# Kernel tuning notes

Hardware: AMD Instinct MI355X
Metric: run time of the kernel (lower is better)

The kernel has to match this reference:

```python
import jax, jax.numpy as jnp
import numpy as np

B, S, D_MODEL, H = 2, 2048, 1024, 16
D_K = D_MODEL // H
THETA = 10000.0


def setup_inputs() -> dict:
    key = jax.random.key(0)
    k1, k2, k3 = jax.random.split(key, 3)
    x = jax.random.normal(k1, (B, S, D_MODEL), dtype=jnp.float32)
    token_positions = jnp.tile(jnp.arange(S, dtype=jnp.int32), (B, 1))
    qkv_w = jax.random.normal(k2, (3 * D_MODEL, D_MODEL), dtype=jnp.float32) * (D_MODEL ** -0.5)
    out_w = jax.random.normal(k3, (D_MODEL, D_MODEL), dtype=jnp.float32) * (D_MODEL ** -0.5)
    return {"x": x, "token_positions": token_positions, "qkv_w": qkv_w, "out_w": out_w}


def _apply_rope(t, pos):
    # t: [B, H, S, d_k], pos: [B, S]
    half = D_K // 2
    inv_freq = THETA ** (-jnp.arange(0, half, dtype=jnp.float32) * 2.0 / D_K)  # [half]
    ang = pos.astype(jnp.float32)[:, None, :, None] * inv_freq  # [B,1,S,half]
    cos, sin = jnp.cos(ang), jnp.sin(ang)
    t1 = t[..., 0::2]
    t2 = t[..., 1::2]
    r1 = t1 * cos - t2 * sin
    r2 = t1 * sin + t2 * cos
    # interleave back: [..., half, 2] -> [..., d_k]
    return jnp.stack([r1, r2], axis=-1).reshape(t.shape)


def reference(x, token_positions, qkv_w, out_w):
    # fused QKV projection (no bias)
    qkv = jnp.einsum('bsd,ed->bse', x, qkv_w)  # [B,S,3*D_MODEL]
    qkv = qkv.reshape(B, S, 3, H, D_K)
    q = jnp.transpose(qkv[:, :, 0], (0, 2, 1, 3))  # [B,H,S,d_k]
    k = jnp.transpose(qkv[:, :, 1], (0, 2, 1, 3))
    v = jnp.transpose(qkv[:, :, 2], (0, 2, 1, 3))
    q = _apply_rope(q, token_positions)
    k = _apply_rope(k, token_positions)
    scores = jnp.einsum('bhqd,bhkd->bhqk', q, k) / jnp.sqrt(jnp.asarray(D_K, x.dtype))
    causal = jnp.tril(jnp.ones((S, S), dtype=bool))
    neg_inf = jnp.finfo(scores.dtype).min
    scores = jnp.where(causal, scores, neg_inf)
    attn = jax.nn.softmax(scores, axis=-1)
    out = jnp.einsum('bhqk,bhkd->bhqd', attn, v)  # [B,H,S,d_k]
    out = jnp.transpose(out, (0, 2, 1, 3)).reshape(B, S, D_MODEL)
    return jnp.einsum('bsd,ed->bse', out, out_w)
```

## Files before the change

### kernel.cpp

```cpp
#include <hip/hip_runtime.h>
#include <cstdint>

typedef unsigned short u16;
typedef unsigned int u32;
typedef __attribute__((ext_vector_type(8))) short short8;
typedef __attribute__((ext_vector_type(4))) float f32x4;

static constexpr int Bc = 2, Sc = 2048, DMc = 1024, Hc = 16, DKc = 64;
static constexpr int Mc = Bc * Sc;

__device__ __forceinline__ float b2f(u16 u) { return __uint_as_float((u32)u << 16); }
__device__ __forceinline__ u16 f2b(float f) {
  u32 x = __float_as_uint(f);
  return (u16)((x + 0x7fffu + ((x >> 16) & 1u)) >> 16);
}
__device__ __forceinline__ u32 pack2(float lo, float hi) {
  return (u32)f2b(lo) | ((u32)f2b(hi) << 16);
}

__global__ __launch_bounds__(256)
void cvt_f32_bf16_k(const float* __restrict__ src, u16* __restrict__ dst, int n8)
{
  const int i = blockIdx.x * 256 + threadIdx.x;
  if (i >= n8) return;
  const float4 a = *(const float4*)(src + (size_t)i * 8);
  const float4 b = *(const float4*)(src + (size_t)i * 8 + 4);
  uint4 o;
  o.x = pack2(a.x, a.y);
  o.y = pack2(a.z, a.w);
  o.z = pack2(b.x, b.y);
  o.w = pack2(b.z, b.w);
  *(uint4*)(dst + (size_t)i * 8) = o;
}

template <typename OutT>
__global__ __launch_bounds__(256, 2)
void gemm_bt128(const u16* __restrict__ A, const u16* __restrict__ W,
                OutT* __restrict__ C, int M, int N, int K)
{
  __shared__ u16 As[128 * 32];
  __shared__ u16 Bs[128 * 32];
  const int t = threadIdx.x;
  const int w = t >> 6, l = t & 63;
  const int wr = w >> 1, wc = w & 1;
  const int l4 = l >> 4, l15 = l & 15;
  const int bm = blockIdx.x, bn = blockIdx.y;

  f32x4 acc[4][4] = {};

  const int rowA = bm * 128, rowB = bn * 128;
  const int sr = l >> 2, sk = (l & 3) * 8;

  for (int k0 = 0; k0 < K; k0 += 32) {
    __syncthreads();
#pragma unroll
    for (int i = 0; i < 2; ++i) {
      const int chunk = i * 4 + w;
      const u16* ga = A + (size_t)(rowA + chunk * 16 + sr) * K + k0 + sk;
      const u16* gb = W + (size_t)(rowB + chunk * 16 + sr) * K + k0 + sk;
      __builtin_amdgcn_global_load_lds((const __attribute__((address_space(1))) void*)ga,
                                       (__attribute__((address_space(3))) void*)(As + chunk * 512), 16, 0, 0);
      __builtin_amdgcn_global_load_lds((const __attribute__((address_space(1))) void*)gb,
                                       (__attribute__((address_space(3))) void*)(Bs + chunk * 512), 16, 0, 0);
    }
    __syncthreads();
    short8 af[4], bf[4];
#pragma unroll
    for (int m = 0; m < 4; ++m)
      af[m] = *(const short8*)(As + (wr * 64 + m * 16 + l15) * 32 + l4 * 8);
#pragma unroll
    for (int n = 0; n < 4; ++n)
      bf[n] = *(const short8*)(Bs + (wc * 64 + n * 16 + l15) * 32 + l4 * 8);
#pragma unroll
    for (int m = 0; m < 4; ++m)
#pragma unroll
      for (int n = 0; n < 4; ++n)
        acc[m][n] = __builtin_amdgcn_mfma_f32_16x16x32_bf16(af[m], bf[n], acc[m][n], 0, 0, 0);
  }

#pragma unroll
  for (int m = 0; m < 4; ++m) {
    const int r0 = rowA + wr * 64 + m * 16 + l4 * 4;
#pragma unroll
    for (int n = 0; n < 4; ++n) {
      const int c0 = rowB + wc * 64 + n * 16 + l15;
#pragma unroll
      for (int r = 0; r < 4; ++r) {
        const float v = acc[m][n][r];
        if constexpr (sizeof(OutT) == 2)
          C[(size_t)(r0 + r) * N + c0] = (OutT)f2b(v);
        else
          C[(size_t)(r0 + r) * N + c0] = (OutT)v;
      }
    }
  }
}

__global__ void rope_table_k(float2* __restrict__ tab)
{
  const int idx = blockIdx.x * 256 + threadIdx.x;
  const int p = idx >> 5, i = idx & 31;
  const float invf = powf(10000.0f, -(float)(2 * i) / 64.0f);
  const float ang = (float)p * invf;
  tab[idx] = make_float2(cosf(ang), sinf(ang));
}

__global__ __launch_bounds__(256)
void rope_reshape_k(const u16* __restrict__ qkv, const int* __restrict__ tokpos,
                    const float2* __restrict__ tab,
                    u16* __restrict__ Q, u16* __restrict__ K, u16* __restrict__ Vt)
{
  __shared__ u16 Vs[64][72];
  const int t = threadIdx.x;
  const int st = blockIdx.x, h = blockIdx.y, b = blockIdx.z;

  {
    const int sl = t >> 2, iq = t & 3;
    const int s = st * 64 + sl;
    const int p = tokpos[b * Sc + s];
    const size_t row = (size_t)(b * Sc + s) * 3 * DMc + h * DKc + iq * 16;
    const size_t orow = ((size_t)(b * Hc + h) * Sc + s) * DKc + iq * 16;
#pragma unroll
    for (int which = 0; which < 2; ++which) {
      const u16* g = qkv + row + which * DMc;
      uint4 va = *(const uint4*)g;
      uint4 vb = *(const uint4*)(g + 8);
      u32 in[8] = {va.x, va.y, va.z, va.w, vb.x, vb.y, vb.z, vb.w};
      const float scale = (which == 0) ? 0.125f : 1.0f;
      u32 ow[8];
#pragma unroll
      for (int j = 0; j < 8; ++j) {
        const float2 cs = tab[p * 32 + iq * 8 + j];
        const float t1 = b2f((u16)(in[j] & 0xffffu));
        const float t2 = b2f((u16)(in[j] >> 16));
        ow[j] = pack2((t1 * cs.x - t2 * cs.y) * scale, (t1 * cs.y + t2 * cs.x) * scale);
      }
      u16* dst = (which == 0 ? Q : K) + orow;
      *(uint4*)dst = make_uint4(ow[0], ow[1], ow[2], ow[3]);
      *(uint4*)(dst + 8) = make_uint4(ow[4], ow[5], ow[6], ow[7]);
    }
  }
#pragma unroll
  for (int it = 0; it < 2; ++it) {
    const int sv = it * 32 + (t >> 3);
    const int d0 = (t & 7) * 8;
    const u16* g = qkv + (size_t)(b * Sc + st * 64 + sv) * 3 * DMc + 2 * DMc + h * DKc + d0;
    *(uint4*)&Vs[sv][d0] = *(const uint4*)g;
  }
  __syncthreads();
  {
    const int d = t >> 2, s0 = (t & 3) * 16;
    u16 tmp[16];
#pragma unroll
    for (int j = 0; j < 16; ++j) tmp[j] = Vs[s0 + j][d];
    u16* dst = Vt + ((size_t)(b * Hc + h) * DKc + d) * Sc + st * 64 + s0;
    *(uint4*)dst = *(const uint4*)tmp;
    *(uint4*)(dst + 8) = *(const uint4*)(tmp + 8);
  }
}

__global__ __launch_bounds__(256, 2)
void attn_k(const u16* __restrict__ Q, const u16* __restrict__ K,
            const u16* __restrict__ Vt, u16* __restrict__ O)
{
  __shared__ u16 Kls[2][64 * 64];
  __shared__ u16 Vls[2][64 * 64];
  __shared__ u16 Psh[4][16 * 64];
  __shared__ float Fsh[4][16];

  const int t = threadIdx.x, w = t >> 6, l = t & 63;
  const int l4 = l >> 4, l15 = l & 15;

  int bid = blockIdx.x + 16 * (blockIdx.y + Hc * blockIdx.z);
  bid = (bid & 7) * 64 + (bid >> 3);
  const int p = bid & 15, h = (bid >> 4) & 15, b = bid >> 8;

  const size_t bh = (size_t)b * Hc + h;
  const u16* Qb = Q + bh * Sc * DKc;
  const u16* Kb = K + bh * Sc * DKc;
  const u16* Vb = Vt + bh * (size_t)DKc * Sc;
  char* Pw = (char*)&Psh[w][0];
  float* Fw = &Fsh[w][0];
  const int swz = (l15 & 7) << 4;

  int srow[2], scol[2];
#pragma unroll
  for (int j = 0; j < 2; ++j) {
    const int e = j * 256 + t;
    srow[j] = e >> 3;
    scol[j] = (((e & 7) * 16) ^ ((srow[j] & 7) << 4)) >> 1;
  }

  auto stage = [&](int buf, int kv0) {
#pragma unroll
    for (int j = 0; j < 2; ++j) {
      const u16* gk = Kb + (size_t)(kv0 + srow[j]) * DKc + scol[j];
      __builtin_amdgcn_global_load_lds((const __attribute__((address_space(1))) void*)gk,
          (__attribute__((address_space(3))) void*)(&Kls[buf][0] + (j * 256 + w * 64) * 8), 16, 0, 0);
    }
#pragma unroll
    for (int j = 0; j < 2; ++j) {
      const u16* gv = Vb + (size_t)srow[j] * Sc + kv0 + scol[j];
      __builtin_amdgcn_global_load_lds((const __attribute__((address_space(1))) void*)gv,
          (__attribute__((address_space(3))) void*)(&Vls[buf][0] + (j * 256 + w * 64) * 8), 16, 0, 0);
    }
  };

#pragma unroll
  for (int seg = 0; seg < 2; ++seg) {
    const int qt = seg ? p : 31 - p;
    const int q0 = qt * 64 + w * 16;
    const int niter = qt + 1;

    const short8 qf0 = *(const short8*)(Qb + (size_t)(q0 + l15) * DKc + l4 * 8);
    const short8 qf1 = *(const short8*)(Qb + (size_t)(q0 + l15) * DKc + 32 + l4 * 8);

    f32x4 o[4] = {};
    float m = -1e30f, lsum = 0.f;

    stage(0, 0);
    for (int it = 0; it < niter; ++it) {
      const int buf = it & 1;
      const int kv0 = it * 64;
      if (it + 1 < niter) {
        stage(buf ^ 1, kv0 + 64);
        asm volatile("s_waitcnt vmcnt(4)" ::: "memory");
      } else {
        asm volatile("s_waitcnt vmcnt(0)" ::: "memory");
      }
      __builtin_amdgcn_s_barrier();

      const char* Kbuf = (const char*)&Kls[buf][0];
      const char* Vbuf = (const char*)&Vls[buf][0];

      f32x4 sc[4];
#pragma unroll
      for (int c = 0; c < 4; ++c) {
        const int rb = (c * 16 + l15) * 128;
        const short8 ka  = *(const short8*)(Kbuf + rb + ((l4 * 16) ^ swz));
        const short8 kb2 = *(const short8*)(Kbuf + rb + ((64 + l4 * 16) ^ swz));
        f32x4 z = {0.f, 0.f, 0.f, 0.f};
        z = __builtin_amdgcn_mfma_f32_16x16x32_bf16(ka, qf0, z, 0, 0, 0);
        z = __builtin_amdgcn_mfma_f32_16x16x32_bf16(kb2, qf1, z, 0, 0, 0);
        sc[c] = z;
      }
      if (kv0 + 63 > q0) {
#pragma unroll
        for (int c = 0; c < 4; ++c) {
          const int kvr = kv0 + c * 16 + l4 * 4;
#pragma unroll
          for (int r = 0; r < 4; ++r)
            if (kvr + r > q0 + l15) sc[c][r] = -1e30f;
        }
      }
      float pmax = -1e30f;
#pragma unroll
      for (int c = 0; c < 4; ++c)
        pmax = fmaxf(pmax, fmaxf(fmaxf(sc[c][0], sc[c][1]), fmaxf(sc[c][2], sc[c][3])));
      pmax = fmaxf(pmax, __shfl_xor(pmax, 16));
      pmax = fmaxf(pmax, __shfl_xor(pmax, 32));
      const float mnew = fmaxf(m, pmax);
      const float fac = __expf(m - mnew);
      float rs = 0.f;
#pragma unroll
      for (int c = 0; c < 4; ++c) {
        const float p0 = __expf(sc[c][0] - mnew);
        const float p1 = __expf(sc[c][1] - mnew);
        const float p2 = __expf(sc[c][2] - mnew);
        const float p3 = __expf(sc[c][3] - mnew);
        rs += (p0 + p1) + (p2 + p3);
        uint2 pk;
        pk.x = pack2(p0, p1);
        pk.y = pack2(p2, p3);
        *(uint2*)(Pw + ((l15 * 128 + c * 32 + l4 * 8) ^ swz)) = pk;
      }
      rs += __shfl_xor(rs, 16);
      rs += __shfl_xor(rs, 32);
      lsum = lsum * fac + rs;
      m = mnew;
      Fw[l15] = fac;
      const f32x4 f4 = *(const f32x4*)&Fw[l4 * 4];
#pragma unroll
      for (int dc = 0; dc < 4; ++dc) {
        o[dc][0] *= f4[0]; o[dc][1] *= f4[1];
        o[dc][2] *= f4[2]; o[dc][3] *= f4[3];
      }
#pragma unroll
      for (int kv2 = 0; kv2 < 2; ++kv2) {
        const short8 pa = *(const short8*)(Pw + ((l15 * 128 + kv2 * 64 + l4 * 16) ^ swz));
#pragma unroll
        for (int dc = 0; dc < 4; ++dc) {
          const short8 vf = *(const short8*)(Vbuf + (dc * 16 + l15) * 128 + ((kv2 * 64 + l4 * 16) ^ swz));
          o[dc] = __builtin_amdgcn_mfma_f32_16x16x32_bf16(pa, vf, o[dc], 0, 0, 0);
        }
      }
      asm volatile("s_waitcnt lgkmcnt(0)" ::: "memory");
      __builtin_amdgcn_s_barrier();
    }
    Fw[l15] = lsum;
    const f32x4 lv = *(const f32x4*)&Fw[l4 * 4];
#pragma unroll
    for (int dc = 0; dc < 4; ++dc) {
      const int col = h * DKc + dc * 16 + l15;
#pragma unroll
      for (int r = 0; r < 4; ++r)
        O[(size_t)(b * Sc + q0 + l4 * 4 + r) * DMc + col] = f2b(o[dc][r] / lv[r]);
    }
  }
}

extern "C" void kernel_launch(void* const* d_in, const int* in_sizes, int n_in,
                              void* d_out, int out_size, void* d_ws, size_t ws_size,
                              hipStream_t stream)
{
  const float* x      = (const float*)d_in[0];
  const int*   tokpos = (const int*)d_in[1];
  const float* qkv_w  = (const float*)d_in[2];
  const float* out_w  = (const float*)d_in[3];
  float* out = (float*)d_out;

  char* ws = (char*)d_ws;
  size_t off = 0;
  u16* xb   = (u16*)(ws + off); off += (size_t)Mc * DMc * 2;
  u16* qwb  = (u16*)(ws + off); off += (size_t)3 * DMc * DMc * 2;
  u16* owb  = (u16*)(ws + off); off += (size_t)DMc * DMc * 2;
  u16* qkv  = (u16*)(ws + off); off += (size_t)Mc * 3 * DMc * 2;
  u16* Qr   = (u16*)(ws + off); off += (size_t)Bc * Hc * Sc * DKc * 2;
  u16* Kr   = (u16*)(ws + off); off += (size_t)Bc * Hc * Sc * DKc * 2;
  u16* Vt   = (u16*)(ws + off); off += (size_t)Bc * Hc * DKc * Sc * 2;
  u16* Oa   = (u16*)(ws + off); off += (size_t)Mc * DMc * 2;
  float2* tab = (float2*)(ws + off); off += (size_t)Sc * 32 * sizeof(float2);

  cvt_f32_bf16_k<<<(Mc * DMc / 8 + 255) / 256, 256, 0, stream>>>(x, xb, Mc * DMc / 8);
  cvt_f32_bf16_k<<<(3 * DMc * DMc / 8 + 255) / 256, 256, 0, stream>>>(qkv_w, qwb, 3 * DMc * DMc / 8);
  cvt_f32_bf16_k<<<(DMc * DMc / 8 + 255) / 256, 256, 0, stream>>>(out_w, owb, DMc * DMc / 8);

  rope_table_k<<<(Sc * 32) / 256, 256, 0, stream>>>(tab);
  gemm_bt128<u16><<<dim3(Mc / 128, 3 * DMc / 128), 256, 0, stream>>>(xb, qwb, qkv, Mc, 3 * DMc, DMc);
  rope_reshape_k<<<dim3(Sc / 64, Hc, Bc), 256, 0, stream>>>(qkv, tokpos, tab, Qr, Kr, Vt);
  attn_k<<<dim3(16, Hc, Bc), 256, 0, stream>>>(Qr, Kr, Vt, Oa);
  gemm_bt128<float><<<dim3(Mc / 128, DMc / 128), 256, 0, stream>>>(Oa, owb, out, Mc, DMc, DMc);
}
```

Baseline: 133.8 us.

## Split attention KV range across two blocks and merge with combine kernel

Attention work is split so each (batch, head, q-pair) is processed by two blocks, each taking alternating 64-wide KV tiles. This doubles the grid to 1024 blocks and raises occupancy to 4 blocks per CU. The P tile is now written into the K LDS buffer instead of a separate shared array, which lowers LDS use per block. Partial outputs and (max, sum) statistics go to fp32 scratch, and a new combine kernel merges them into bf16. The three conversion kernels are also fused into one launch, and workspace buffers are aliased. The cost is extra global traffic for the partial outputs plus one more launch.

```diff
diff --git a/kernel.cpp b/kernel.cpp
--- a/kernel.cpp
+++ b/kernel.cpp
@@ -8,6 +8,7 @@
 
 static constexpr int Bc = 2, Sc = 2048, DMc = 1024, Hc = 16, DKc = 64;
 static constexpr int Mc = Bc * Sc;
+static constexpr int BHSc = Bc * Hc * Sc;
 
 __device__ __forceinline__ float b2f(u16 u) { return __uint_as_float((u32)u << 16); }
 __device__ __forceinline__ u16 f2b(float f) {
@@ -19,18 +20,23 @@
 }
 
 __global__ __launch_bounds__(256)
-void cvt_f32_bf16_k(const float* __restrict__ src, u16* __restrict__ dst, int n8)
+void cvt3_k(const float* __restrict__ x, const float* __restrict__ qw,
+            const float* __restrict__ ow,
+            u16* __restrict__ xb, u16* __restrict__ qwb, u16* __restrict__ owb)
 {
   const int i = blockIdx.x * 256 + threadIdx.x;
-  if (i >= n8) return;
-  const float4 a = *(const float4*)(src + (size_t)i * 8);
-  const float4 b = *(const float4*)(src + (size_t)i * 8 + 4);
+  const float* src; u16* dst; int j;
+  if (i < 524288)      { src = x;  dst = xb;  j = i; }
+  else if (i < 917504) { src = qw; dst = qwb; j = i - 524288; }
+  else                 { src = ow; dst = owb; j = i - 917504; }
+  const float4 a = *(const float4*)(src + (size_t)j * 8);
+  const float4 b = *(const float4*)(src + (size_t)j * 8 + 4);
   uint4 o;
   o.x = pack2(a.x, a.y);
   o.y = pack2(a.z, a.w);
   o.z = pack2(b.x, b.y);
   o.w = pack2(b.z, b.w);
-  *(uint4*)(dst + (size_t)i * 8) = o;
+  *(uint4*)(dst + (size_t)j * 8) = o;
 }
 
 template <typename OutT>
@@ -159,29 +165,36 @@
   }
 }
 
-__global__ __launch_bounds__(256, 2)
+__global__ __launch_bounds__(256, 4)
 void attn_k(const u16* __restrict__ Q, const u16* __restrict__ K,
-            const u16* __restrict__ Vt, u16* __restrict__ O)
+            const u16* __restrict__ Vt, float* __restrict__ Opart,
+            float2* __restrict__ ML)
 {
   __shared__ u16 Kls[2][64 * 64];
   __shared__ u16 Vls[2][64 * 64];
-  __shared__ u16 Psh[4][16 * 64];
-  __shared__ float Fsh[4][16];
 
   const int t = threadIdx.x, w = t >> 6, l = t & 63;
   const int l4 = l >> 4, l15 = l & 15;
 
-  int bid = blockIdx.x + 16 * (blockIdx.y + Hc * blockIdx.z);
-  bid = (bid & 7) * 64 + (bid >> 3);
-  const int p = bid & 15, h = (bid >> 4) & 15, b = bid >> 8;
-
-  const size_t bh = (size_t)b * Hc + h;
-  const u16* Qb = Q + bh * Sc * DKc;
-  const u16* Kb = K + bh * Sc * DKc;
-  const u16* Vb = Vt + bh * (size_t)DKc * Sc;
-  char* Pw = (char*)&Psh[w][0];
-  float* Fw = &Fsh[w][0];
+  int bid = blockIdx.x;
+  bid = (bid & 7) * 128 + (bid >> 3);
+  const int p = bid & 15, part = (bid >> 4) & 1, h = (bid >> 5) & 15, b = bid >> 9;
+
+  const int bh = b * Hc + h;
+  const u16* Qb = Q + (size_t)bh * Sc * DKc;
+  const u16* Kb = K + (size_t)bh * Sc * DKc;
+  const u16* Vb = Vt + (size_t)bh * DKc * Sc;
   const int swz = (l15 & 7) << 4;
+
+  const int qt0 = 31 - p, qt1 = p;
+  const int q00 = qt0 * 64 + w * 16, q01 = qt1 * 64 + w * 16;
+  const int n0 = (qt0 + 2 - part) >> 1, n1 = (qt1 + 2 - part) >> 1;
+  const int ntot = n0 + n1;
+
+  const short8 qf0a = *(const short8*)(Qb + (size_t)(q00 + l15) * DKc + l4 * 8);
+  const short8 qf0b = *(const short8*)(Qb + (size_t)(q00 + l15) * DKc + 32 + l4 * 8);
+  const short8 qf1a = *(const short8*)(Qb + (size_t)(q01 + l15) * DKc + l4 * 8);
+  const short8 qf1b = *(const short8*)(Qb + (size_t)(q01 + l15) * DKc + 32 + l4 * 8);
 
   int srow[2], scol[2];
 #pragma unroll
@@ -190,7 +203,6 @@
     srow[j] = e >> 3;
     scol[j] = (((e & 7) * 16) ^ ((srow[j] & 7) << 4)) >> 1;
   }
-
   auto stage = [&](int buf, int kv0) {
 #pragma unroll
     for (int j = 0; j < 2; ++j) {
@@ -205,108 +217,146 @@
           (__attribute__((address_space(3))) void*)(&Vls[buf][0] + (j * 256 + w * 64) * 8), 16, 0, 0);
     }
   };
-
-#pragma unroll
-  for (int seg = 0; seg < 2; ++seg) {
-    const int qt = seg ? p : 31 - p;
-    const int q0 = qt * 64 + w * 16;
-    const int niter = qt + 1;
-
-    const short8 qf0 = *(const short8*)(Qb + (size_t)(q0 + l15) * DKc + l4 * 8);
-    const short8 qf1 = *(const short8*)(Qb + (size_t)(q0 + l15) * DKc + 32 + l4 * 8);
-
-    f32x4 o[4] = {};
-    float m = -1e30f, lsum = 0.f;
-
-    stage(0, 0);
-    for (int it = 0; it < niter; ++it) {
-      const int buf = it & 1;
-      const int kv0 = it * 64;
-      if (it + 1 < niter) {
-        stage(buf ^ 1, kv0 + 64);
-        asm volatile("s_waitcnt vmcnt(4)" ::: "memory");
-      } else {
-        asm volatile("s_waitcnt vmcnt(0)" ::: "memory");
+  auto kvof = [&](int i) {
+    return ((i < n0) ? (part + 2 * i) : (part + 2 * (i - n0))) * 64;
+  };
+
+  f32x4 o[4] = {};
+  float m = -1e30f, lsum = 0.f;
+  int qcur = q00;
+  short8 qfA = qf0a, qfB = qf0b;
+
+  auto epi = [&](int qbase) {
+    const size_t pbase = ((size_t)part * Bc * Hc + bh) * Sc;
+    if (l < 16) ML[pbase + qbase + l15] = make_float2(m, lsum);
+#pragma unroll
+    for (int dc = 0; dc < 4; ++dc)
+#pragma unroll
+      for (int r = 0; r < 4; ++r)
+        Opart[(pbase + qbase + l4 * 4 + r) * 64 + dc * 16 + l15] = o[dc][r];
+  };
+
+  stage(0, kvof(0));
+  for (int i = 0; i < ntot; ++i) {
+    const int buf = i & 1;
+    const int kv0 = kvof(i);
+    if (i + 1 < ntot) {
+      stage(buf ^ 1, kvof(i + 1));
+      asm volatile("s_waitcnt vmcnt(4)" ::: "memory");
+    } else {
+      asm volatile("s_waitcnt vmcnt(0)" ::: "memory");
+    }
+    __builtin_amdgcn_s_barrier();
+
+    const char* Kbuf = (const char*)&Kls[buf][0];
+    const char* Vbuf = (const char*)&Vls[buf][0];
+    char* Pw = (char*)&Kls[buf][0] + w * 2048;
+
+    f32x4 sc[4];
+#pragma unroll
+    for (int c = 0; c < 4; ++c) {
+      const int rb = (c * 16 + l15) * 128;
+      const short8 ka  = *(const short8*)(Kbuf + rb + ((l4 * 16) ^ swz));
+      const short8 kb2 = *(const short8*)(Kbuf + rb + ((64 + l4 * 16) ^ swz));
+      f32x4 z = {0.f, 0.f, 0.f, 0.f};
+      z = __builtin_amdgcn_mfma_f32_16x16x32_bf16(ka, qfA, z, 0, 0, 0);
+      z = __builtin_amdgcn_mfma_f32_16x16x32_bf16(kb2, qfB, z, 0, 0, 0);
+      sc[c] = z;
+    }
+    if (kv0 + 63 > qcur) {
+#pragma unroll
+      for (int c = 0; c < 4; ++c) {
+        const int kvr = kv0 + c * 16 + l4 * 4;
+#pragma unroll
+        for (int r = 0; r < 4; ++r)
+          if (kvr + r > qcur + l15) sc[c][r] = -1e30f;
       }
-      __builtin_amdgcn_s_barrier();
-
-      const char* Kbuf = (const char*)&Kls[buf][0];
-      const char* Vbuf = (const char*)&Vls[buf][0];
-
-      f32x4 sc[4];
-#pragma unroll
-      for (int c = 0; c < 4; ++c) {
-        const int rb = (c * 16 + l15) * 128;
-        const short8 ka  = *(const short8*)(Kbuf + rb + ((l4 * 16) ^ swz));
-        const short8 kb2 = *(const short8*)(Kbuf + rb + ((64 + l4 * 16) ^ swz));
-        f32x4 z = {0.f, 0.f, 0.f, 0.f};
-        z = __builtin_amdgcn_mfma_f32_16x16x32_bf16(ka, qf0, z, 0, 0, 0);
-        z = __builtin_amdgcn_mfma_f32_16x16x32_bf16(kb2, qf1, z, 0, 0, 0);
-        sc[c] = z;
+    }
+    float pmax = -1e30f;
+#pragma unroll
+    for (int c = 0; c < 4; ++c)
+      pmax = fmaxf(pmax, fmaxf(fmaxf(sc[c][0], sc[c][1]), fmaxf(sc[c][2], sc[c][3])));
+    pmax = fmaxf(pmax, __shfl_xor(pmax, 16));
+    pmax = fmaxf(pmax, __shfl_xor(pmax, 32));
+    const float mnew = fmaxf(m, pmax);
+    const float fac = __expf(m - mnew);
+    float rs = 0.f;
+    u32 pk[4][2];
+#pragma unroll
+    for (int c = 0; c < 4; ++c) {
+      const float p0 = __expf(sc[c][0] - mnew);
+      const float p1 = __expf(sc[c][1] - mnew);
+      const float p2 = __expf(sc[c][2] - mnew);
+      const float p3 = __expf(sc[c][3] - mnew);
+      rs += (p0 + p1) + (p2 + p3);
+      pk[c][0] = pack2(p0, p1);
+      pk[c][1] = pack2(p2, p3);
+    }
+    rs += __shfl_xor(rs, 16);
+    rs += __shfl_xor(rs, 32);
+    lsum = lsum * fac + rs;
+    m = mnew;
+
+    asm volatile("s_waitcnt lgkmcnt(0)" ::: "memory");
+    __builtin_amdgcn_s_barrier();
+
+#pragma unroll
+    for (int c = 0; c < 4; ++c) {
+      uint2 u; u.x = pk[c][0]; u.y = pk[c][1];
+      *(uint2*)(Pw + ((l15 * 128 + c * 32 + l4 * 8) ^ swz)) = u;
+    }
+    float f4[4];
+#pragma unroll
+    for (int r = 0; r < 4; ++r) f4[r] = __shfl(fac, l4 * 4 + r);
+#pragma unroll
+    for (int dc = 0; dc < 4; ++dc) {
+      o[dc][0] *= f4[0]; o[dc][1] *= f4[1];
+      o[dc][2] *= f4[2]; o[dc][3] *= f4[3];
+    }
+#pragma unroll
+    for (int kv2 = 0; kv2 < 2; ++kv2) {
+      const short8 pa = *(const short8*)(Pw + ((l15 * 128 + kv2 * 64 + l4 * 16) ^ swz));
+#pragma unroll
+      for (int dc = 0; dc < 4; ++dc) {
+        const short8 vf = *(const short8*)(Vbuf + (dc * 16 + l15) * 128 + ((kv2 * 64 + l4 * 16) ^ swz));
+        o[dc] = __builtin_amdgcn_mfma_f32_16x16x32_bf16(pa, vf, o[dc], 0, 0, 0);
       }
-      if (kv0 + 63 > q0) {
-#pragma unroll
-        for (int c = 0; c < 4; ++c) {
-          const int kvr = kv0 + c * 16 + l4 * 4;
-#pragma unroll
-          for (int r = 0; r < 4; ++r)
-            if (kvr + r > q0 + l15) sc[c][r] = -1e30f;
-        }
-      }
-      float pmax = -1e30f;
-#pragma unroll
-      for (int c = 0; c < 4; ++c)
-        pmax = fmaxf(pmax, fmaxf(fmaxf(sc[c][0], sc[c][1]), fmaxf(sc[c][2], sc[c][3])));
-      pmax = fmaxf(pmax, __shfl_xor(pmax, 16));
-      pmax = fmaxf(pmax, __shfl_xor(pmax, 32));
-      const float mnew = fmaxf(m, pmax);
-      const float fac = __expf(m - mnew);
-      float rs = 0.f;
-#pragma unroll
-      for (int c = 0; c < 4; ++c) {
-        const float p0 = __expf(sc[c][0] - mnew);
-        const float p1 = __expf(sc[c][1] - mnew);
-        const float p2 = __expf(sc[c][2] - mnew);
-        const float p3 = __expf(sc[c][3] - mnew);
-        rs += (p0 + p1) + (p2 + p3);
-        uint2 pk;
-        pk.x = pack2(p0, p1);
-        pk.y = pack2(p2, p3);
-        *(uint2*)(Pw + ((l15 * 128 + c * 32 + l4 * 8) ^ swz)) = pk;
-      }
-      rs += __shfl_xor(rs, 16);
-      rs += __shfl_xor(rs, 32);
-      lsum = lsum * fac + rs;
-      m = mnew;
-      Fw[l15] = fac;
-      const f32x4 f4 = *(const f32x4*)&Fw[l4 * 4];
-#pragma unroll
-      for (int dc = 0; dc < 4; ++dc) {
-        o[dc][0] *= f4[0]; o[dc][1] *= f4[1];
-        o[dc][2] *= f4[2]; o[dc][3] *= f4[3];
-      }
-#pragma unroll
-      for (int kv2 = 0; kv2 < 2; ++kv2) {
-        const short8 pa = *(const short8*)(Pw + ((l15 * 128 + kv2 * 64 + l4 * 16) ^ swz));
-#pragma unroll
-        for (int dc = 0; dc < 4; ++dc) {
-          const short8 vf = *(const short8*)(Vbuf + (dc * 16 + l15) * 128 + ((kv2 * 64 + l4 * 16) ^ swz));
-          o[dc] = __builtin_amdgcn_mfma_f32_16x16x32_bf16(pa, vf, o[dc], 0, 0, 0);
-        }
-      }
-      asm volatile("s_waitcnt lgkmcnt(0)" ::: "memory");
-      __builtin_amdgcn_s_barrier();
-    }
-    Fw[l15] = lsum;
-    const f32x4 lv = *(const f32x4*)&Fw[l4 * 4];
-#pragma unroll
-    for (int dc = 0; dc < 4; ++dc) {
-      const int col = h * DKc + dc * 16 + l15;
-#pragma unroll
-      for (int r = 0; r < 4; ++r)
-        O[(size_t)(b * Sc + q0 + l4 * 4 + r) * DMc + col] = f2b(o[dc][r] / lv[r]);
-    }
-  }
+    }
+    asm volatile("s_waitcnt lgkmcnt(0)" ::: "memory");
+    __builtin_amdgcn_s_barrier();
+
+    if (i == n0 - 1) {
+      epi(q00);
+#pragma unroll
+      for (int dc = 0; dc < 4; ++dc) o[dc] = f32x4{0.f, 0.f, 0.f, 0.f};
+      m = -1e30f; lsum = 0.f;
+      qcur = q01; qfA = qf1a; qfB = qf1b;
+    }
+  }
+  epi(q01);
+}
+
+__global__ __launch_bounds__(256)
+void combine_k(const float* __restrict__ Opart, const float2* __restrict__ ML,
+               u16* __restrict__ Oa)
+{
+  const int idx = blockIdx.x * 256 + threadIdx.x;
+  const int row = idx >> 4, c4 = idx & 15;
+  const float2 a = ML[row], bm = ML[BHSc + row];
+  const float m = fmaxf(a.x, bm.x);
+  const float w0 = __expf(a.x - m), w1 = __expf(bm.x - m);
+  const float inv = 1.0f / (w0 * a.y + w1 * bm.y);
+  const float4 o0 = *(const float4*)(Opart + (size_t)row * 64 + c4 * 4);
+  const float4 o1 = *(const float4*)(Opart + ((size_t)BHSc + row) * 64 + c4 * 4);
+  const float r0 = (w0 * o0.x + w1 * o1.x) * inv;
+  const float r1 = (w0 * o0.y + w1 * o1.y) * inv;
+  const float r2 = (w0 * o0.z + w1 * o1.z) * inv;
+  const float r3 = (w0 * o0.w + w1 * o1.w) * inv;
+  const int s = row & (Sc - 1), bh = row >> 11, b = bh >> 4, h = bh & 15;
+  uint2 pk;
+  pk.x = pack2(r0, r1);
+  pk.y = pack2(r2, r3);
+  *(uint2*)(Oa + ((size_t)(b * Sc + s) * DMc + h * DKc + c4 * 4)) = pk;
 }
 
 extern "C" void kernel_launch(void* const* d_in, const int* in_sizes, int n_in,
@@ -321,23 +371,24 @@
 
   char* ws = (char*)d_ws;
   size_t off = 0;
-  u16* xb   = (u16*)(ws + off); off += (size_t)Mc * DMc * 2;
-  u16* qwb  = (u16*)(ws + off); off += (size_t)3 * DMc * DMc * 2;
-  u16* owb  = (u16*)(ws + off); off += (size_t)DMc * DMc * 2;
-  u16* qkv  = (u16*)(ws + off); off += (size_t)Mc * 3 * DMc * 2;
-  u16* Qr   = (u16*)(ws + off); off += (size_t)Bc * Hc * Sc * DKc * 2;
-  u16* Kr   = (u16*)(ws + off); off += (size_t)Bc * Hc * Sc * DKc * 2;
-  u16* Vt   = (u16*)(ws + off); off += (size_t)Bc * Hc * DKc * Sc * 2;
-  u16* Oa   = (u16*)(ws + off); off += (size_t)Mc * DMc * 2;
+  u16*   qkv   = (u16*)(ws + off);
+  u16*   xb    = (u16*)(ws + off + 25165824);
+  u16*   qwb   = (u16*)(ws + off + 33554432);
+  float* Opart = (float*)(ws + off);
+  float2* ML   = (float2*)(ws + off + 33554432);
+  off += 39845888;
+  u16* owb = (u16*)(ws + off); off += (size_t)DMc * DMc * 2;
+  u16* Qr  = (u16*)(ws + off); off += (size_t)Bc * Hc * Sc * DKc * 2;
+  u16* Kr  = (u16*)(ws + off); off += (size_t)Bc * Hc * Sc * DKc * 2;
+  u16* Vt  = (u16*)(ws + off); off += (size_t)Bc * Hc * DKc * Sc * 2;
+  u16* Oa  = (u16*)(ws + off); off += (size_t)Mc * DMc * 2;
   float2* tab = (float2*)(ws + off); off += (size_t)Sc * 32 * sizeof(float2);
 
-  cvt_f32_bf16_k<<<(Mc * DMc / 8 + 255) / 256, 256, 0, stream>>>(x, xb, Mc * DMc / 8);
-  cvt_f32_bf16_k<<<(3 * DMc * DMc / 8 + 255) / 256, 256, 0, stream>>>(qkv_w, qwb, 3 * DMc * DMc / 8);
-  cvt_f32_bf16_k<<<(DMc * DMc / 8 + 255) / 256, 256, 0, stream>>>(out_w, owb, DMc * DMc / 8);
-
+  cvt3_k<<<4096, 256, 0, stream>>>(x, qkv_w, out_w, xb, qwb, owb);
   rope_table_k<<<(Sc * 32) / 256, 256, 0, stream>>>(tab);
   gemm_bt128<u16><<<dim3(Mc / 128, 3 * DMc / 128), 256, 0, stream>>>(xb, qwb, qkv, Mc, 3 * DMc, DMc);
   rope_reshape_k<<<dim3(Sc / 64, Hc, Bc), 256, 0, stream>>>(qkv, tokpos, tab, Qr, Kr, Vt);
-  attn_k<<<dim3(16, Hc, Bc), 256, 0, stream>>>(Qr, Kr, Vt, Oa);
+  attn_k<<<1024, 256, 0, stream>>>(Qr, Kr, Vt, Opart, ML);
+  combine_k<<<BHSc * 16 / 256, 256, 0, stream>>>(Opart, ML, Oa);
   gemm_bt128<float><<<dim3(Mc / 128, DMc / 128), 256, 0, stream>>>(Oa, owb, out, Mc, DMc, DMc);
 }
```

Result: no change. 134.5 us (+0.5%).
